# Performance work log

Hardware: AMD Instinct MI355X
Metric: run time of the kernel (lower is better)

Reference implementation:

```python
import jax, jax.numpy as jnp
import numpy as np

DIM = 512
NUM_HEADS = 8
B, NW, W = 8, 64, 64  # batch, num_windows, window_size


def setup_inputs() -> dict:
    key = jax.random.key(0)
    k1, k2, k3 = jax.random.split(key, 3)
    x = jax.random.normal(k1, (B, NW, W, DIM), dtype=jnp.float32)
    w_qkv = jax.random.normal(k2, (DIM, 3 * DIM), dtype=jnp.float32) * (DIM ** -0.5)
    w_proj = jax.random.normal(k3, (DIM, DIM), dtype=jnp.float32) * (DIM ** -0.5)
    b_proj = jnp.zeros((DIM,), dtype=jnp.float32)
    return {"x": x, "w_qkv": w_qkv, "w_proj": w_proj, "b_proj": b_proj}


def reference(x, w_qkv, w_proj, b_proj):
    batch, nw, w, dim = x.shape
    heads = NUM_HEADS
    dh = dim // heads
    scale = dh ** -0.5
    # qkv projection (no bias): [B, nW, W, 3*dim]
    qkv = jnp.einsum('bnwc,cd->bnwd', x, w_qkv)
    # -> [B, nW, W, 3, H, dh] -> [3, B, H, nW, W, dh]
    qkv = qkv.reshape(batch, nw, w, 3, heads, dh)
    qkv = jnp.transpose(qkv, (3, 0, 4, 1, 2, 5))
    q, k, v = qkv[0], qkv[1], qkv[2]
    # attention logits per window: [B, H, nW, W, W]
    attn = jnp.einsum('bhnqd,bhnkd->bhnqk', q, k) * scale
    attn = jax.nn.softmax(attn, axis=-1)
    # [B, H, nW, W, dh]
    out = jnp.einsum('bhnqk,bhnkd->bhnqd', attn, v)
    # faithful raw reshape (no transpose), matching the TF source
    out = out.reshape(batch, nw, w, dim)
    return jnp.einsum('bnwc,cd->bnwd', out, w_proj) + b_proj
```

## Files before the change

### kernel.cpp

```cpp
#include <hip/hip_runtime.h>
#include <hip/hip_bf16.h>

typedef __bf16 bf16_t;
typedef __bf16 bf16x8 __attribute__((ext_vector_type(8)));
typedef float f32x4 __attribute__((ext_vector_type(4)));
typedef float f32x16 __attribute__((ext_vector_type(16)));

#define GLOAD_LDS16(gp, lp) __builtin_amdgcn_global_load_lds( \
    (const __attribute__((address_space(1))) void*)(gp),      \
    (__attribute__((address_space(3))) void*)(lp), 16, 0, 0)

__device__ __forceinline__ int swz64(int row, int col) {
    return row * 64 + (col ^ ((row & 7) << 3));
}

__global__ __launch_bounds__(256) void transpose_cast_kernel(
    const float* __restrict__ src, bf16_t* __restrict__ dst, int R, int C)
{
    __shared__ float tile[32][33];
    const int bx = blockIdx.x;
    const int by = blockIdx.y;
    const int t  = threadIdx.x;
    const int i0 = t >> 5;
    const int j  = t & 31;
#pragma unroll
    for (int p = 0; p < 4; ++p) {
        int i = i0 + p * 8;
        tile[i][j] = src[(long)(by * 32 + i) * C + bx * 32 + j];
    }
    __syncthreads();
#pragma unroll
    for (int p = 0; p < 4; ++p) {
        int i = i0 + p * 8;
        dst[(long)(bx * 32 + i) * R + by * 32 + j] = (bf16_t)tile[j][i];
    }
}

__global__ __launch_bounds__(256, 2) void qkv_attn_kernel(
    const float*  __restrict__ x,
    const bf16_t* __restrict__ wT,
    bf16_t* __restrict__ ao)
{
    __shared__ bf16_t arena[32768];
    bf16_t* const lX = arena;
    bf16_t* const lW = arena + 8192;

    const int id   = blockIdx.x;
    const int xcd  = id & 7;
    const int s    = id >> 3;
    const int pr   = xcd * 32 + (s >> 3);
    const int h    = s & 7;
    const int wid0 = pr * 2;

    const float* xw = x + (long)wid0 * 64 * 512;

    const int t    = threadIdx.x;
    const int wv   = t >> 6;
    const int lane = t & 63;
    const int wm   = wv >> 1;
    const int wn   = wv & 1;
    const int l31  = lane & 31;
    const int l5   = lane >> 5;

    bf16_t* const lQw = arena +     0 + wm * 12288;
    bf16_t* const lKw = arena +  4096 + wm * 12288;
    bf16_t* const lVw = arena +  8192 + wm * 12288;
    bf16_t* const lPw = arena + 24576 + wm * 4096;

    f32x16 acc[2][3];
#pragma unroll
    for (int mi = 0; mi < 2; ++mi)
#pragma unroll
        for (int ni = 0; ni < 3; ++ni) acc[mi][ni] = (f32x16)0.0f;

    for (int kc = 0; kc < 8; ++kc) {
        const int k0 = kc * 64;
#pragma unroll
        for (int p = 0; p < 4; ++p) {
            const int v  = t + p * 256;
            const int r  = v >> 3;
            const int sl = v & 7;
            const float* rp = xw + (long)r * 512 + k0 + sl * 8;
            f32x4 f0 = *(const f32x4*)rp;
            f32x4 f1 = *(const f32x4*)(rp + 4);
            bf16x8 o;
            o[0] = (bf16_t)f0[0]; o[1] = (bf16_t)f0[1];
            o[2] = (bf16_t)f0[2]; o[3] = (bf16_t)f0[3];
            o[4] = (bf16_t)f1[0]; o[5] = (bf16_t)f1[1];
            o[6] = (bf16_t)f1[2]; o[7] = (bf16_t)f1[3];
            *(bf16x8*)&lX[r * 64 + ((sl ^ (r & 7)) * 8)] = o;
        }
        {
            const int lsub = lane >> 3;
            const int sl   = lane & 7;
#pragma unroll
            for (int j = 0; j < 6; ++j) {
                const int rb   = wv * 6 + j;
                const int nr   = rb * 8 + lsub;
                const int ch   = sl ^ (nr & 7);
                const int grow = ((nr >> 6) << 9) + h * 64 + (nr & 63);
                GLOAD_LDS16(wT + (long)grow * 512 + k0 + ch * 8, &lW[rb * 512]);
            }
        }
        __syncthreads();
#pragma unroll
        for (int ks = 0; ks < 64; ks += 16) {
            bf16x8 a0 = *(const bf16x8*)&lX[swz64(wm * 64 +  0 + l31, ks + l5 * 8)];
            bf16x8 a1 = *(const bf16x8*)&lX[swz64(wm * 64 + 32 + l31, ks + l5 * 8)];
#pragma unroll
            for (int ni = 0; ni < 3; ++ni) {
                bf16x8 b = *(const bf16x8*)&lW[swz64(wn * 96 + ni * 32 + l31, ks + l5 * 8)];
                acc[0][ni] = __builtin_amdgcn_mfma_f32_32x32x16_bf16(a0, b, acc[0][ni], 0, 0, 0);
                acc[1][ni] = __builtin_amdgcn_mfma_f32_32x32x16_bf16(a1, b, acc[1][ni], 0, 0, 0);
            }
        }
        __syncthreads();
    }

#pragma unroll
    for (int mi = 0; mi < 2; ++mi) {
#pragma unroll
        for (int ni = 0; ni < 3; ++ni) {
            const int n = wn * 96 + ni * 32 + l31;
            const int g = n >> 6;
            const int c = n & 63;
#pragma unroll
            for (int r = 0; r < 16; ++r) {
                const int tk = mi * 32 + (r & 3) + ((r >> 2) << 3) + (l5 << 2);
                const bf16_t val = (bf16_t)acc[mi][ni][r];
                if (g == 0)      lQw[swz64(tk, c)] = val;
                else if (g == 1) lKw[swz64(tk, c)] = val;
                else             lVw[swz64(c, tk)] = val;
            }
        }
    }
    __syncthreads();

    const int lr = lane & 15;
    const int q  = lane >> 4;
    const int qh = wn * 32;
    const float scale = 0.125f;

    f32x4 sA[2][4];
#pragma unroll
    for (int i = 0; i < 2; ++i)
#pragma unroll
        for (int j = 0; j < 4; ++j) sA[i][j] = (f32x4)0.0f;
#pragma unroll
    for (int ks = 0; ks < 64; ks += 32) {
        bf16x8 aq0 = *(const bf16x8*)&lQw[swz64(qh +  0 + lr, ks + q * 8)];
        bf16x8 aq1 = *(const bf16x8*)&lQw[swz64(qh + 16 + lr, ks + q * 8)];
#pragma unroll
        for (int j = 0; j < 4; ++j) {
            bf16x8 bk = *(const bf16x8*)&lKw[swz64(j * 16 + lr, ks + q * 8)];
            sA[0][j] = __builtin_amdgcn_mfma_f32_16x16x32_bf16(aq0, bk, sA[0][j], 0, 0, 0);
            sA[1][j] = __builtin_amdgcn_mfma_f32_16x16x32_bf16(aq1, bk, sA[1][j], 0, 0, 0);
        }
    }

#pragma unroll
    for (int i = 0; i < 2; ++i)
#pragma unroll
    for (int reg = 0; reg < 4; ++reg) {
        float m = fmaxf(fmaxf(sA[i][0][reg], sA[i][1][reg]),
                        fmaxf(sA[i][2][reg], sA[i][3][reg]));
#pragma unroll
        for (int d = 1; d < 16; d <<= 1) m = fmaxf(m, __shfl_xor(m, d));
        float p[4];
        float sum = 0.0f;
#pragma unroll
        for (int j = 0; j < 4; ++j) {
            p[j] = __expf((sA[i][j][reg] - m) * scale);
            sum += p[j];
        }
#pragma unroll
        for (int d = 1; d < 16; d <<= 1) sum += __shfl_xor(sum, d);
        const float inv = 1.0f / sum;
        const int row = qh + i * 16 + q * 4 + reg;
#pragma unroll
        for (int j = 0; j < 4; ++j)
            lPw[swz64(row, j * 16 + lr)] = (bf16_t)(p[j] * inv);
    }

    f32x4 o[2][4];
#pragma unroll
    for (int i = 0; i < 2; ++i)
#pragma unroll
        for (int d4 = 0; d4 < 4; ++d4) o[i][d4] = (f32x4)0.0f;
#pragma unroll
    for (int ks = 0; ks < 64; ks += 32) {
        bf16x8 ap0 = *(const bf16x8*)&lPw[swz64(qh +  0 + lr, ks + q * 8)];
        bf16x8 ap1 = *(const bf16x8*)&lPw[swz64(qh + 16 + lr, ks + q * 8)];
#pragma unroll
        for (int d4 = 0; d4 < 4; ++d4) {
            bf16x8 bv = *(const bf16x8*)&lVw[swz64(d4 * 16 + lr, ks + q * 8)];
            o[0][d4] = __builtin_amdgcn_mfma_f32_16x16x32_bf16(ap0, bv, o[0][d4], 0, 0, 0);
            o[1][d4] = __builtin_amdgcn_mfma_f32_16x16x32_bf16(ap1, bv, o[1][d4], 0, 0, 0);
        }
    }

    const int wid = wid0 + wm;
    const int bb  = wid >> 6;
    const int nw  = wid & 63;
    bf16_t* aop = ao + ((long)bb * 4096 + (long)h * 512 + nw * 8) * 512;
#pragma unroll
    for (int i = 0; i < 2; ++i)
#pragma unroll
    for (int d4 = 0; d4 < 4; ++d4)
#pragma unroll
    for (int reg = 0; reg < 4; ++reg) {
        const int wr = qh + i * 16 + q * 4 + reg;
        aop[(long)(wr >> 3) * 512 + (wr & 7) * 64 + d4 * 16 + lr] =
            (bf16_t)o[i][d4][reg];
    }
}

#define LDP 72

__global__ __launch_bounds__(256) void gemm2_kernel(
    const bf16_t* __restrict__ A,
    const bf16_t* __restrict__ Bt,
    const float*  __restrict__ bias,
    float* __restrict__ C,
    int M, int N, int K)
{
    __shared__ bf16_t lA[128 * LDP];
    __shared__ bf16_t lB[128 * LDP];

    const int tid  = threadIdx.x;
    const int wave = tid >> 6;
    const int lane = tid & 63;
    const int wm   = wave >> 1;
    const int wn   = wave & 1;
    const int lr   = lane & 15;
    const int q    = lane >> 4;

    const int id  = blockIdx.x;
    const int xcd = id & 7;
    const int s   = id >> 3;
    const int bm  = xcd * 32 + (s >> 2);
    const int bn  = s & 3;

    const long arow0 = (long)bm * 128;
    const long brow0 = (long)bn * 128;

    f32x4 acc[4][4];
#pragma unroll
    for (int i = 0; i < 4; ++i)
#pragma unroll
        for (int j = 0; j < 4; ++j) acc[i][j] = (f32x4)0.0f;

    const int srow = tid >> 3;
    const int scol = (tid & 7) * 8;

    const int nk = K / 64;
    for (int kt = 0; kt < nk; ++kt) {
        const bf16_t* Ag = A + arow0 * K + kt * 64;
        const bf16_t* Bg = Bt + brow0 * K + kt * 64;
        bf16x8 av[4], bv[4];
#pragma unroll
        for (int p = 0; p < 4; ++p) {
            const int r = srow + p * 32;
            av[p] = *(const bf16x8*)(Ag + (long)r * K + scol);
            bv[p] = *(const bf16x8*)(Bg + (long)r * K + scol);
        }
#pragma unroll
        for (int p = 0; p < 4; ++p) {
            const int r = srow + p * 32;
            *(bf16x8*)&lA[r * LDP + scol] = av[p];
            *(bf16x8*)&lB[r * LDP + scol] = bv[p];
        }
        __syncthreads();
#pragma unroll
        for (int ks = 0; ks < 64; ks += 32) {
            bf16x8 af[4], bf[4];
#pragma unroll
            for (int i = 0; i < 4; ++i)
                af[i] = *(const bf16x8*)&lA[(wm * 64 + i * 16 + lr) * LDP + ks + q * 8];
#pragma unroll
            for (int j = 0; j < 4; ++j)
                bf[j] = *(const bf16x8*)&lB[(wn * 64 + j * 16 + lr) * LDP + ks + q * 8];
#pragma unroll
            for (int i = 0; i < 4; ++i)
#pragma unroll
                for (int j = 0; j < 4; ++j)
                    acc[i][j] = __builtin_amdgcn_mfma_f32_16x16x32_bf16(
                        af[i], bf[j], acc[i][j], 0, 0, 0);
        }
        __syncthreads();
    }

#pragma unroll
    for (int i = 0; i < 4; ++i) {
        const long r = arow0 + wm * 64 + i * 16 + q * 4;
#pragma unroll
        for (int j = 0; j < 4; ++j) {
            const long c = brow0 + wn * 64 + j * 16 + lr;
            const float bv2 = bias[c];
#pragma unroll
            for (int reg = 0; reg < 4; ++reg) {
                C[(r + reg) * N + c] = acc[i][j][reg] + bv2;
            }
        }
    }
}

extern "C" void kernel_launch(void* const* d_in, const int* in_sizes, int n_in,
                              void* d_out, int out_size, void* d_ws, size_t ws_size,
                              hipStream_t stream)
{
    (void)in_sizes; (void)n_in; (void)out_size; (void)ws_size;
    const float* x     = (const float*)d_in[0];
    const float* wqkv  = (const float*)d_in[1];
    const float* wproj = (const float*)d_in[2];
    const float* bproj = (const float*)d_in[3];
    float* out = (float*)d_out;

    bf16_t* wT = (bf16_t*)d_ws;
    bf16_t* pT = wT + (size_t)1536 * 512;
    bf16_t* ao = pT + (size_t)512 * 512;

    transpose_cast_kernel<<<dim3(48, 16), 256, 0, stream>>>(wqkv, wT, 512, 1536);
    transpose_cast_kernel<<<dim3(16, 16), 256, 0, stream>>>(wproj, pT, 512, 512);

    qkv_attn_kernel<<<2048, 256, 0, stream>>>(x, wT, ao);

    gemm2_kernel<<<1024, 256, 0, stream>>>(
        ao, pT, bproj, out, 32768, 512, 512);
}
```

Measured before the change: 234.3 us.

## Pre-cast x to bf16, double-buffer QKV staging via global_load_lds, swizzle gemm2 LDS

Adds a separate kernel that casts x to bf16 once, so the fused QKV/attention kernel can stage x directly into LDS with async global_load_lds instead of loading fp32 and converting in registers. The QKV GEMM loop becomes double-buffered, loading the next k-chunk while computing the current one, and LDS grows to 80KB. gemm2 also switches to direct-to-LDS loads with an XOR-swizzled layout in place of padded rows. The cost is an extra full pass over x (a 64MB fp32 read plus a 32MB bf16 write) and higher LDS use, which may limit the two-blocks-per-CU occupancy target.

```diff
diff --git a/kernel.cpp b/kernel.cpp
--- a/kernel.cpp
+++ b/kernel.cpp
@@ -36,14 +36,32 @@
     }
 }
 
+__global__ __launch_bounds__(256) void cast_x_kernel(
+    const float* __restrict__ src, bf16_t* __restrict__ dst, long n8)
+{
+    long i = (long)blockIdx.x * blockDim.x + threadIdx.x;
+    const long stride = (long)gridDim.x * blockDim.x;
+    for (; i < n8; i += stride) {
+        const float* p = src + i * 8;
+        f32x4 f0 = *(const f32x4*)p;
+        f32x4 f1 = *(const f32x4*)(p + 4);
+        bf16x8 o;
+        o[0] = (bf16_t)f0[0]; o[1] = (bf16_t)f0[1];
+        o[2] = (bf16_t)f0[2]; o[3] = (bf16_t)f0[3];
+        o[4] = (bf16_t)f1[0]; o[5] = (bf16_t)f1[1];
+        o[6] = (bf16_t)f1[2]; o[7] = (bf16_t)f1[3];
+        *(bf16x8*)(dst + i * 8) = o;
+    }
+}
+
 __global__ __launch_bounds__(256, 2) void qkv_attn_kernel(
-    const float*  __restrict__ x,
+    const bf16_t* __restrict__ xb,
     const bf16_t* __restrict__ wT,
     bf16_t* __restrict__ ao)
 {
-    __shared__ bf16_t arena[32768];
-    bf16_t* const lX = arena;
-    bf16_t* const lW = arena + 8192;
+    __shared__ bf16_t arena[40960];
+    bf16_t* const buf0 = arena;
+    bf16_t* const buf1 = arena + 20480;
 
     const int id   = blockIdx.x;
     const int xcd  = id & 7;
@@ -52,7 +70,7 @@
     const int h    = s & 7;
     const int wid0 = pr * 2;
 
-    const float* xw = x + (long)wid0 * 64 * 512;
+    const bf16_t* xw = xb + (long)wid0 * 64 * 512;
 
     const int t    = threadIdx.x;
     const int wv   = t >> 6;
@@ -61,48 +79,38 @@
     const int wn   = wv & 1;
     const int l31  = lane & 31;
     const int l5   = lane >> 5;
+    const int rlo  = lane >> 3;
+    const int ch   = (lane & 7) ^ rlo;
 
     bf16_t* const lQw = arena +     0 + wm * 12288;
     bf16_t* const lKw = arena +  4096 + wm * 12288;
     bf16_t* const lVw = arena +  8192 + wm * 12288;
     bf16_t* const lPw = arena + 24576 + wm * 4096;
 
+    auto stage = [&](bf16_t* buf, int k0) {
+#pragma unroll
+        for (int p = 0; p < 4; ++p) {
+            const int rb = wv * 4 + p;
+            GLOAD_LDS16(xw + (long)(rb * 8 + rlo) * 512 + k0 + ch * 8,
+                        buf + rb * 512);
+        }
+#pragma unroll
+        for (int j = 0; j < 6; ++j) {
+            const int rb = wv * 6 + j;
+            const int nr = rb * 8 + rlo;
+            const int grow = ((nr >> 6) << 9) + h * 64 + (nr & 63);
+            GLOAD_LDS16(wT + (long)grow * 512 + k0 + ch * 8,
+                        buf + 8192 + rb * 512);
+        }
+    };
+
     f32x16 acc[2][3];
 #pragma unroll
     for (int mi = 0; mi < 2; ++mi)
 #pragma unroll
         for (int ni = 0; ni < 3; ++ni) acc[mi][ni] = (f32x16)0.0f;
 
-    for (int kc = 0; kc < 8; ++kc) {
-        const int k0 = kc * 64;
-#pragma unroll
-        for (int p = 0; p < 4; ++p) {
-            const int v  = t + p * 256;
-            const int r  = v >> 3;
-            const int sl = v & 7;
-            const float* rp = xw + (long)r * 512 + k0 + sl * 8;
-            f32x4 f0 = *(const f32x4*)rp;
-            f32x4 f1 = *(const f32x4*)(rp + 4);
-            bf16x8 o;
-            o[0] = (bf16_t)f0[0]; o[1] = (bf16_t)f0[1];
-            o[2] = (bf16_t)f0[2]; o[3] = (bf16_t)f0[3];
-            o[4] = (bf16_t)f1[0]; o[5] = (bf16_t)f1[1];
-            o[6] = (bf16_t)f1[2]; o[7] = (bf16_t)f1[3];
-            *(bf16x8*)&lX[r * 64 + ((sl ^ (r & 7)) * 8)] = o;
-        }
-        {
-            const int lsub = lane >> 3;
-            const int sl   = lane & 7;
-#pragma unroll
-            for (int j = 0; j < 6; ++j) {
-                const int rb   = wv * 6 + j;
-                const int nr   = rb * 8 + lsub;
-                const int ch   = sl ^ (nr & 7);
-                const int grow = ((nr >> 6) << 9) + h * 64 + (nr & 63);
-                GLOAD_LDS16(wT + (long)grow * 512 + k0 + ch * 8, &lW[rb * 512]);
-            }
-        }
-        __syncthreads();
+    auto compute = [&](const bf16_t* lX, const bf16_t* lW) {
 #pragma unroll
         for (int ks = 0; ks < 64; ks += 16) {
             bf16x8 a0 = *(const bf16x8*)&lX[swz64(wm * 64 +  0 + l31, ks + l5 * 8)];
@@ -114,6 +122,18 @@
                 acc[1][ni] = __builtin_amdgcn_mfma_f32_32x32x16_bf16(a1, b, acc[1][ni], 0, 0, 0);
             }
         }
+    };
+
+    stage(buf0, 0);
+    __syncthreads();
+#pragma unroll 1
+    for (int kc2 = 0; kc2 < 4; ++kc2) {
+        const int kc = kc2 * 2;
+        stage(buf1, (kc + 1) * 64);
+        compute(buf0, buf0 + 8192);
+        __syncthreads();
+        if (kc + 2 < 8) stage(buf0, (kc + 2) * 64);
+        compute(buf1, buf1 + 8192);
         __syncthreads();
     }
 
@@ -215,8 +235,6 @@
     }
 }
 
-#define LDP 72
-
 __global__ __launch_bounds__(256) void gemm2_kernel(
     const bf16_t* __restrict__ A,
     const bf16_t* __restrict__ Bt,
@@ -224,8 +242,8 @@
     float* __restrict__ C,
     int M, int N, int K)
 {
-    __shared__ bf16_t lA[128 * LDP];
-    __shared__ bf16_t lB[128 * LDP];
+    __shared__ bf16_t lA[8192];
+    __shared__ bf16_t lB[8192];
 
     const int tid  = threadIdx.x;
     const int wave = tid >> 6;
@@ -234,6 +252,8 @@
     const int wn   = wave & 1;
     const int lr   = lane & 15;
     const int q    = lane >> 4;
+    const int rlo  = lane >> 3;
+    const int ch   = (lane & 7) ^ rlo;
 
     const int id  = blockIdx.x;
     const int xcd = id & 7;
@@ -250,25 +270,15 @@
 #pragma unroll
         for (int j = 0; j < 4; ++j) acc[i][j] = (f32x4)0.0f;
 
-    const int srow = tid >> 3;
-    const int scol = (tid & 7) * 8;
-
     const int nk = K / 64;
     for (int kt = 0; kt < nk; ++kt) {
-        const bf16_t* Ag = A + arow0 * K + kt * 64;
-        const bf16_t* Bg = Bt + brow0 * K + kt * 64;
-        bf16x8 av[4], bv[4];
+        const long k0 = kt * 64;
 #pragma unroll
         for (int p = 0; p < 4; ++p) {
-            const int r = srow + p * 32;
-            av[p] = *(const bf16x8*)(Ag + (long)r * K + scol);
-            bv[p] = *(const bf16x8*)(Bg + (long)r * K + scol);
-        }
-#pragma unroll
-        for (int p = 0; p < 4; ++p) {
-            const int r = srow + p * 32;
-            *(bf16x8*)&lA[r * LDP + scol] = av[p];
-            *(bf16x8*)&lB[r * LDP + scol] = bv[p];
+            const int rb = wave * 4 + p;
+            const int r  = rb * 8 + rlo;
+            GLOAD_LDS16(A  + (arow0 + r) * (long)K + k0 + ch * 8, lA + rb * 512);
+            GLOAD_LDS16(Bt + (brow0 + r) * (long)K + k0 + ch * 8, lB + rb * 512);
         }
         __syncthreads();
 #pragma unroll
@@ -276,10 +286,10 @@
             bf16x8 af[4], bf[4];
 #pragma unroll
             for (int i = 0; i < 4; ++i)
-                af[i] = *(const bf16x8*)&lA[(wm * 64 + i * 16 + lr) * LDP + ks + q * 8];
+                af[i] = *(const bf16x8*)&lA[swz64(wm * 64 + i * 16 + lr, ks + q * 8)];
 #pragma unroll
             for (int j = 0; j < 4; ++j)
-                bf[j] = *(const bf16x8*)&lB[(wn * 64 + j * 16 + lr) * LDP + ks + q * 8];
+                bf[j] = *(const bf16x8*)&lB[swz64(wn * 64 + j * 16 + lr, ks + q * 8)];
 #pragma unroll
             for (int i = 0; i < 4; ++i)
 #pragma unroll
@@ -309,7 +319,7 @@
                               void* d_out, int out_size, void* d_ws, size_t ws_size,
                               hipStream_t stream)
 {
-    (void)in_sizes; (void)n_in; (void)out_size; (void)ws_size;
+    (void)in_sizes; (void)n_in; (void)out_size;
     const float* x     = (const float*)d_in[0];
     const float* wqkv  = (const float*)d_in[1];
     const float* wproj = (const float*)d_in[2];
@@ -320,10 +330,18 @@
     bf16_t* pT = wT + (size_t)1536 * 512;
     bf16_t* ao = pT + (size_t)512 * 512;
 
+    const size_t base_elems = (size_t)1536 * 512 + (size_t)512 * 512
+                            + (size_t)32768 * 512;
+    const size_t xb_elems   = (size_t)32768 * 512;
+    bf16_t* xb = (ws_size >= (base_elems + xb_elems) * sizeof(bf16_t))
+               ? (ao + xb_elems)
+               : (bf16_t*)d_out;
+
     transpose_cast_kernel<<<dim3(48, 16), 256, 0, stream>>>(wqkv, wT, 512, 1536);
     transpose_cast_kernel<<<dim3(16, 16), 256, 0, stream>>>(wproj, pT, 512, 512);
-
-    qkv_attn_kernel<<<2048, 256, 0, stream>>>(x, wT, ao);
+    cast_x_kernel<<<2048, 256, 0, stream>>>(x, xb, (long)32768 * 512 / 8);
+
+    qkv_attn_kernel<<<2048, 256, 0, stream>>>(xb, wT, ao);
 
     gemm2_kernel<<<1024, 256, 0, stream>>>(
         ao, pT, bproj, out, 32768, 512, 512);
```

Result: faster. 228.7 us (-2.4%).
